# Kernel tuning notes

Measured on AMD Instinct MI355X. Metric: run time of the kernel, lower is better.

The kernel has to match this reference:

```python
import jax, jax.numpy as jnp
import numpy as np

H, I, C, B, T = 128, 270, 3, 1024, 270


def setup_inputs() -> dict:
    key = jax.random.key(0)
    ks = jax.random.split(key, 6)
    inp = {
        "x": jax.random.normal(ks[0], (B, T, I), dtype=jnp.float32),
        "Wf": jax.random.normal(ks[1], (H, I + H), dtype=jnp.float32) * 0.01,
        "Wi": jax.random.normal(ks[2], (H, I + H), dtype=jnp.float32) * 0.01,
        "Wc": jax.random.normal(ks[3], (H, I + H), dtype=jnp.float32) * 0.01,
        "Wo": jax.random.normal(ks[4], (H, I + H), dtype=jnp.float32) * 0.01,
        "Wy": jax.random.normal(ks[5], (C, H), dtype=jnp.float32) * 0.01,
        "bf": jnp.zeros((H,), jnp.float32),
        "bi": jnp.zeros((H,), jnp.float32),
        "bc": jnp.zeros((H,), jnp.float32),
        "bo": jnp.zeros((H,), jnp.float32),
        "by": jnp.zeros((C,), jnp.float32),
    }
    return inp


def _lstm_forward(x, Wf, Wi, Wc, Wo, Wy, bf, bi, bc, bo, by):
    # combined = [h_prev, x_t], so W[:, :H] acts on h, W[:, H:] acts on x.
    Wh = jnp.stack([Wf[:, :H], Wi[:, :H], Wc[:, :H], Wo[:, :H]])      # [4,H,H]
    Wx = jnp.stack([Wf[:, H:], Wi[:, H:], Wc[:, H:], Wo[:, H:]])      # [4,H,I]
    b = jnp.stack([bf, bi, bc, bo])                                   # [4,H]
    # Precompute input projections for all timesteps: one big GEMM.
    xp = jnp.einsum('bti,ghi->tbgh', x, Wx)                           # [T,B,4,H]

    def step(carry, xpt):
        h, c = carry
        pre = xpt + jnp.einsum('bh,gkh->bgk', h, Wh) + b              # [B,4,H]
        f = jax.nn.sigmoid(pre[:, 0])
        i = jax.nn.sigmoid(pre[:, 1])
        g = jnp.tanh(pre[:, 2])
        o = jax.nn.sigmoid(pre[:, 3])
        c_new = f * c + i * g
        h_new = o * jnp.tanh(c_new)
        return (h_new, c_new), h_new

    h0 = jnp.zeros((x.shape[0], H), x.dtype)
    c0 = jnp.zeros((x.shape[0], H), x.dtype)
    _, hs = jax.lax.scan(step, (h0, c0), xp)                          # hs: [T,B,H]
    all_hiddens = jnp.transpose(hs, (1, 0, 2))                        # [B,T,H]
    logits = jnp.einsum('bth,ch->btc', all_hiddens, Wy) + by
    all_outputs = jax.nn.softmax(logits, axis=-1)                     # [B,T,C]
    return all_hiddens, all_outputs


def reference(x, Wf, Wi, Wc, Wo, Wy, bf, bi, bc, bo, by):
    return _lstm_forward(x, Wf, Wi, Wc, Wo, Wy, bf, bi, bc, bo, by)
```

## Files before the change

kernel.cpp:

```cpp
#include <hip/hip_runtime.h>
#include <stdint.h>


typedef __attribute__((ext_vector_type(8))) short short8;
typedef __attribute__((ext_vector_type(4))) float f32x4;
typedef __attribute__((ext_vector_type(2))) float f32x2;
typedef __attribute__((ext_vector_type(4))) unsigned int uint4v;
typedef __attribute__((ext_vector_type(2))) unsigned int u32x2;
typedef unsigned short ush;

#define LOG2E 1.4426950408889634f
#define TWOLOG2E 2.8853900817779268f

__device__ __forceinline__ ush f2bf(float f) {
    unsigned u = __float_as_uint(f);
    return (ush)((u + 0x7FFFu + ((u >> 16) & 1u)) >> 16);
}
__device__ __forceinline__ void lds_barrier() {
    asm volatile("s_waitcnt lgkmcnt(0)" ::: "memory");
    __builtin_amdgcn_s_barrier();
    __builtin_amdgcn_sched_barrier(0);
    asm volatile("" ::: "memory");
}

__global__ __launch_bounds__(256) void pack_w(
    const float* __restrict__ Wf, const float* __restrict__ Wi,
    const float* __restrict__ Wc, const float* __restrict__ Wo,
    const float* __restrict__ bf_, const float* __restrict__ bi_,
    const float* __restrict__ bc_, const float* __restrict__ bo_,
    ush* __restrict__ Wxp, ush* __restrict__ Whp, float* __restrict__ bpk)
{
    int idx = blockIdx.x * 256 + threadIdx.x;
    if (idx < 512 * 288) {
        int u = idx / 288, i = idx - u * 288;
        int g = u >> 7, j = u & 127;
        const float* Wg = (g == 0) ? Wf : (g == 1) ? Wi : (g == 2) ? Wc : Wo;
        float v = (i < 270) ? Wg[(size_t)j * 398 + 128 + i] * LOG2E : 0.f;
        Wxp[idx] = f2bf(v);
    }
    if (idx < 512 * 128) {
        int u = idx >> 7, k = idx & 127;
        int g = u >> 7, j = u & 127;
        const float* Wg = (g == 0) ? Wf : (g == 1) ? Wi : (g == 2) ? Wc : Wo;
        Whp[idx] = f2bf(Wg[(size_t)j * 398 + k] * LOG2E);
    }
    if (idx < 512) {
        int g = idx >> 7, j = idx & 127;
        const float* bg = (g == 0) ? bf_ : (g == 1) ? bi_ : (g == 2) ? bc_ : bo_;
        bpk[idx] = bg[j] * LOG2E;
    }
}

__global__ __launch_bounds__(256, 2) void xp_gemm(
    const float* __restrict__ x, const ush* __restrict__ Wxp,
    const float* __restrict__ bpk, ush* __restrict__ xpc, int t0)
{
    __shared__ ush A_lds[64 * 296];
    const int tid = threadIdx.x;
    const int l = tid & 63, w = tid >> 6;
    const int l16 = l & 15, lq = l >> 4;
    const size_t row0 = (size_t)blockIdx.x * 64;

    const int srow = tid >> 2, sgrp = tid & 3;
    const int r = (int)row0 + srow;
    const int b = r & 1023, tt = (r >> 10) + t0;
    const float* xrow = x + ((size_t)b * 270 + tt) * 270;
    f32x2 stg[9][4];
    #pragma unroll
    for (int ks = 0; ks < 9; ++ks) {
        const int col = ks * 32 + sgrp * 8;
        const float* p = xrow + col;
        if (col + 8 <= 270) {
            stg[ks][0] = *(const f32x2*)p;       stg[ks][1] = *(const f32x2*)(p + 2);
            stg[ks][2] = *(const f32x2*)(p + 4); stg[ks][3] = *(const f32x2*)(p + 6);
        } else {
            float tv[8];
            #pragma unroll
            for (int j = 0; j < 8; ++j) tv[j] = (col + j < 270) ? p[j] : 0.f;
            stg[ks][0] = (f32x2){tv[0], tv[1]}; stg[ks][1] = (f32x2){tv[2], tv[3]};
            stg[ks][2] = (f32x2){tv[4], tv[5]}; stg[ks][3] = (f32x2){tv[6], tv[7]};
        }
    }

    const ush* bptr = Wxp + ((size_t)(w * 128 + l16)) * 288 + lq * 8;
    short8 bA[8], bB[8];
    #pragma unroll
    for (int nt = 0; nt < 8; ++nt) bA[nt] = *(const short8*)(bptr + nt * 4608);
    float bias_v[8];
    #pragma unroll
    for (int nt = 0; nt < 8; ++nt) bias_v[nt] = bpk[w * 128 + nt * 16 + l16];

    {
        ush* wrow = &A_lds[srow * 296 + sgrp * 8];
        #pragma unroll
        for (int ks = 0; ks < 9; ++ks) {
            uint4v o;
            #pragma unroll
            for (int p2 = 0; p2 < 4; ++p2) {
                unsigned v;
                asm("v_cvt_pk_bf16_f32 %0, %1, %2"
                    : "=v"(v) : "v"(stg[ks][p2].x), "v"(stg[ks][p2].y));
                o[p2] = v;
            }
            *(uint4v*)(wrow + ks * 32) = o;
        }
    }
    lds_barrier();

    f32x4 acc[4][8];
    #pragma unroll
    for (int mt = 0; mt < 4; ++mt)
        #pragma unroll
        for (int nt = 0; nt < 8; ++nt)
            acc[mt][nt] = (f32x4){bias_v[nt], bias_v[nt], bias_v[nt], bias_v[nt]};

    #pragma unroll
    for (int ks = 0; ks < 9; ++ks) {
        short8* cur = (ks & 1) ? bB : bA;
        short8* nxt = (ks & 1) ? bA : bB;
        if (ks + 1 < 9) {
            const ush* np = bptr + (ks + 1) * 32;
            #pragma unroll
            for (int nt = 0; nt < 8; ++nt) nxt[nt] = *(const short8*)(np + nt * 4608);
        }
        short8 afr[4];
        #pragma unroll
        for (int mt = 0; mt < 4; ++mt)
            afr[mt] = *(const short8*)(&A_lds[(mt * 16 + l16) * 296 + ks * 32 + lq * 8]);
        #pragma unroll
        for (int mt = 0; mt < 4; ++mt)
            #pragma unroll
            for (int nt = 0; nt < 8; ++nt)
                acc[mt][nt] = __builtin_amdgcn_mfma_f32_16x16x32_bf16(
                    afr[mt], cur[nt], acc[mt][nt], 0, 0, 0);
    }

    const int tloc = (int)(row0 >> 10);
    const int bg0 = ((int)row0 & 1023) >> 4;
    #pragma unroll
    for (int mt = 0; mt < 4; ++mt)
        #pragma unroll
        for (int nt = 0; nt < 8; ++nt) {
            int u = w * 128 + nt * 16 + l16;
            ush* dst = xpc + ((size_t)(tloc * 64 + bg0 + mt) * 512 + u) * 16 + lq * 4;
            #pragma unroll
            for (int q = 0; q < 4; ++q) dst[q] = f2bf(acc[mt][nt][q]);
        }
}

#define STEPB(T, PS, XP, CUR)                                                   \
  {                                                                             \
    const int t_ = (T);                                                         \
    const bool lw_ = (((w >> 2) ^ (t_ & 1)) == 0) && (t_ > t0);                 \
    short8 afr[4];                                                              \
    _Pragma("unroll") for (int kf = 0; kf < 4; ++kf)                            \
      afr[kf] = *(const short8*)(hbase + (CUR) * 4096 + oaf[kf]);               \
    f32x4 acc_[4];                                                              \
    _Pragma("unroll") for (int g = 0; g < 4; ++g) {                             \
      u32x2 pv_ = PS[g];                                                        \
      acc_[g][0] = __uint_as_float(pv_.x << 16);                                \
      acc_[g][1] = __uint_as_float(pv_.x & 0xffff0000u);                        \
      acc_[g][2] = __uint_as_float(pv_.y << 16);                                \
      acc_[g][3] = __uint_as_float(pv_.y & 0xffff0000u);                        \
    }                                                                           \
    if (t_ + 2 < t1) {                                                          \
      _Pragma("unroll") for (int g = 0; g < 4; ++g)                             \
        PS[g] = *(const u32x2*)((XP) + go[g]);                                  \
    }                                                                           \
    (XP) += 2 * TSTEP;                                                          \
    _Pragma("unroll") for (int kf = 0; kf < 4; ++kf)                            \
      _Pragma("unroll") for (int g = 0; g < 4; ++g)                             \
        acc_[g] = __builtin_amdgcn_mfma_f32_16x16x32_bf16(                      \
            afr[kf], whf[g][kf], acc_[g], 0, 0, 0);                             \
    f32x4 ay_ = (f32x4){0.f, 0.f, 0.f, 0.f};                                    \
    if (lw_) {                            \
      ay_ = __builtin_amdgcn_mfma_f32_16x16x32_bf16(afr[0], wyf[0], ay_, 0, 0, 0); \
      ay_ = __builtin_amdgcn_mfma_f32_16x16x32_bf16(afr[1], wyf[1], ay_, 0, 0, 0); \
      ay_ = __builtin_amdgcn_mfma_f32_16x16x32_bf16(afr[2], wyf[2], ay_, 0, 0, 0); \
      ay_ = __builtin_amdgcn_mfma_f32_16x16x32_bf16(afr[3], wyf[3], ay_, 0, 0, 0); \
    }                                                                           \
    _Pragma("unroll") for (int q = 0; q < 4; ++q) {                             \
      float pf_ = __builtin_amdgcn_fmed3f(acc_[0][q], -28.f, 28.f);             \
      float pi_ = __builtin_amdgcn_fmed3f(acc_[1][q], -28.f, 28.f);             \
      float pc2_ = __builtin_amdgcn_fmed3f(acc_[2][q] + acc_[2][q], -28.f, 28.f); \
      float po_ = __builtin_amdgcn_fmed3f(acc_[3][q], -28.f, 28.f);             \
      float ef_ = __builtin_amdgcn_exp2f(-pf_);                                 \
      float ei_ = __builtin_amdgcn_exp2f(-pi_);                                 \
      float ec2_ = __builtin_amdgcn_exp2f(-pc2_);                               \
      float eo_ = __builtin_amdgcn_exp2f(-po_);                                 \
      float df_ = 1.f + ef_;                                                    \
      float di_ = 1.f + ei_;                                                    \
      float dc_ = 1.f + ec2_;                                                   \
      float do2_ = 1.f + eo_;                                                   \
      float didc_ = di_ * dc_;                                                  \
      float num_ = c[q] * didc_ + (1.f - ec2_) * df_;                           \
      float cn_ = num_ * __builtin_amdgcn_rcpf(df_ * didc_);                    \
      c[q] = cn_;                                                               \
      float t2_ = __builtin_amdgcn_fmed3f(cn_, -10.f, 10.f);                    \
      float et2_ = __builtin_amdgcn_exp2f(-TWOLOG2E * t2_);                     \
      float hv_ = (1.f - et2_) * __builtin_amdgcn_rcpf(do2_ * (1.f + et2_));    \
      *(ush*)(hbase + ((CUR) ^ 1) * 4096 + ohw[q]) = f2bf(hv_);                 \
      *op[q] = hv_;                                                             \
      op[q] += 128;                                                             \
    }                                                                           \
    lds_barrier();                                                              \
       \
    if (lw_) {                                                                  \
      int ww_ = w & 3;                                                          \
      float L_ = ((ww_ == 0) ? ay_[0] : (ww_ == 1) ? ay_[1] : (ww_ == 2) ? ay_[2] : ay_[3]) + byl; \
      if (l16 >= 3) L_ = -1e30f;                                                \
      float m_ = fmaxf(L_, __shfl_xor(L_, 1));                                  \
      m_ = fmaxf(m_, __shfl_xor(m_, 2));                                        \
      float e_ = (l16 < 3) ? __expf(L_ - m_) : 0.f;                             \
      float s_ = e_ + __shfl_xor(e_, 1);                                        \
      s_ = s_ + __shfl_xor(s_, 2);                                              \
      if (l16 < 3)                                                              \
        out1[((size_t)(b0 + lq * 4 + ww_) * 270 + (t_ - 1)) * 3 + l16] = e_ * __builtin_amdgcn_rcpf(s_); \
    }                                                                           \
  }

__global__ __launch_bounds__(512) void lstm_scan(
    const ush* __restrict__ xpc, const ush* __restrict__ Whp,
    float* __restrict__ c_state, float* __restrict__ out0, float* __restrict__ out1,
    const float* __restrict__ Wy, const float* __restrict__ by, int t0, int t1)
{
    __shared__ ush h_lds[2][16 * 128];
    const int tid = threadIdx.x;
    const int l = tid & 63, w = tid >> 6;
    const int l16 = l & 15, lq = l >> 4;
    const int b0 = blockIdx.x * 16;
    const int jcol = w * 16 + l16;
    char* hbase = (char*)&h_lds[0][0];

    short8 whf[4][4];
    #pragma unroll
    for (int g = 0; g < 4; ++g) {
        const ush* bw = Whp + ((size_t)(g * 128 + jcol)) * 128 + lq * 8;
        #pragma unroll
        for (int kf = 0; kf < 4; ++kf) whf[g][kf] = *(const short8*)(bw + kf * 32);
    }
    short8 wyf[4];
    #pragma unroll
    for (int kf = 0; kf < 4; ++kf) {
        short8 fr;
        #pragma unroll
        for (int j = 0; j < 8; ++j)
            fr[j] = (l16 < 3) ? (short)f2bf(Wy[l16 * 128 + kf * 32 + lq * 8 + j]) : (short)0;
        wyf[kf] = fr;
    }
    const float byl = (l16 < 3) ? by[l16] : 0.f;

    int oaf[4], ohw[4];
    #pragma unroll
    for (int kf = 0; kf < 4; ++kf)
        oaf[kf] = ((l16 * 128 + kf * 32 + lq * 8) * 2) ^ ((l16 & 7) << 4);
    #pragma unroll
    for (int q = 0; q < 4; ++q) {
        int rr = lq * 4 + q;
        ohw[q] = ((rr * 128 + jcol) * 2) ^ ((rr & 7) << 4);
    }
    float* op[4];
    #pragma unroll
    for (int q = 0; q < 4; ++q)
        op[q] = out0 + (size_t)(b0 + lq * 4 + q) * (270 * 128) + (size_t)t0 * 128 + jcol;

    {
        ush* hp = &h_lds[0][0];
        for (int idx = tid; idx < 2 * 16 * 128; idx += 512) hp[idx] = 0;
    }
    __syncthreads();

    float c[4] = {0.f, 0.f, 0.f, 0.f};
    if (t0 != 0) {
        #pragma unroll
        for (int q = 0; q < 4; ++q)
            c[q] = c_state[(size_t)(b0 + lq * 4 + q) * 128 + jcol];
        for (int idx = tid; idx < 2048; idx += 512) {
            int rr = idx >> 7, k = idx & 127;
            float hvv = out0[(size_t)(b0 + rr) * (270 * 128) + (size_t)(t0 - 1) * 128 + k];
            int off = ((rr * 128 + k) * 2) ^ ((rr & 7) << 4);
            *(ush*)(hbase + off) = f2bf(hvv);
        }
        __syncthreads();
    }

    const size_t TSTEP = (size_t)64 * 512 * 16;
    const ush* xb = xpc + (size_t)blockIdx.x * 8192;
    int go[4];
    #pragma unroll
    for (int g = 0; g < 4; ++g) go[g] = (g * 128 + jcol) * 16 + lq * 4;

    u32x2 Pa[4], Pb[4];
    #pragma unroll
    for (int g = 0; g < 4; ++g) Pa[g] = *(const u32x2*)(xb + go[g]);
    #pragma unroll
    for (int g = 0; g < 4; ++g) Pb[g] = *(const u32x2*)(xb + TSTEP + go[g]);
    const ush* xpa = xb + 2 * TSTEP;
    const ush* xpb = xb + 3 * TSTEP;

    for (int t = t0; t < t1; t += 2) {
        STEPB(t, Pa, xpa, 0)
        STEPB(t + 1, Pb, xpb, 1)
    }

    {
        short8 afr[4];
        #pragma unroll
        for (int kf = 0; kf < 4; ++kf)
            afr[kf] = *(const short8*)(hbase + oaf[kf]);
        if (w < 4) {
            f32x4 ay = (f32x4){0.f, 0.f, 0.f, 0.f};
            ay = __builtin_amdgcn_mfma_f32_16x16x32_bf16(afr[0], wyf[0], ay, 0, 0, 0);
            ay = __builtin_amdgcn_mfma_f32_16x16x32_bf16(afr[1], wyf[1], ay, 0, 0, 0);
            ay = __builtin_amdgcn_mfma_f32_16x16x32_bf16(afr[2], wyf[2], ay, 0, 0, 0);
            ay = __builtin_amdgcn_mfma_f32_16x16x32_bf16(afr[3], wyf[3], ay, 0, 0, 0);
            float L = ((w == 0) ? ay[0] : (w == 1) ? ay[1] : (w == 2) ? ay[2] : ay[3]) + byl;
            if (l16 >= 3) L = -1e30f;
            float m = fmaxf(L, __shfl_xor(L, 1));
            m = fmaxf(m, __shfl_xor(m, 2));
            float e = (l16 < 3) ? __expf(L - m) : 0.f;
            float s = e + __shfl_xor(e, 1);
            s = s + __shfl_xor(s, 2);
            if (l16 < 3)
                out1[((size_t)(b0 + lq * 4 + w) * 270 + (t1 - 1)) * 3 + l16] =
                    e * __builtin_amdgcn_rcpf(s);
        }
    }

    if (t1 != 270) {
        #pragma unroll
        for (int q = 0; q < 4; ++q)
            c_state[(size_t)(b0 + lq * 4 + q) * 128 + jcol] = c[q];
    }
}

extern "C" void kernel_launch(void* const* d_in, const int* in_sizes, int n_in,
                              void* d_out, int out_size, void* d_ws, size_t ws_size,
                              hipStream_t stream) {
    (void)in_sizes; (void)n_in; (void)out_size;
    const float* x   = (const float*)d_in[0];
    const float* Wf  = (const float*)d_in[1];
    const float* Wi  = (const float*)d_in[2];
    const float* Wc  = (const float*)d_in[3];
    const float* Wo  = (const float*)d_in[4];
    const float* Wy  = (const float*)d_in[5];
    const float* bfp = (const float*)d_in[6];
    const float* bip = (const float*)d_in[7];
    const float* bcp = (const float*)d_in[8];
    const float* bop = (const float*)d_in[9];
    const float* byp = (const float*)d_in[10];

    float* out0 = (float*)d_out;
    float* out1 = out0 + (size_t)1024 * 270 * 128;

    long tc = 6;
    {
        const long cand[6] = {270, 90, 54, 30, 18, 6};
        for (int i = 0; i < 6; ++i) {
            size_t need = (size_t)cand[i] * 1048576u + (2u << 20);
            if (need <= ws_size) { tc = cand[i]; break; }
        }
    }
    char* wsb = (char*)d_ws;
    ush* xpc = (ush*)wsb;
    char* fx = wsb + (size_t)tc * 1048576u;
    float* c_state = (float*)fx;
    ush* Wxp = (ush*)(fx + 524288);
    ush* Whp = (ush*)(fx + 524288 + 294912);
    float* bpk = (float*)(fx + 524288 + 294912 + 131072);

    pack_w<<<576, 256, 0, stream>>>(Wf, Wi, Wc, Wo, bfp, bip, bcp, bop, Wxp, Whp, bpk);

    for (int t0 = 0; t0 < 270; t0 += (int)tc) {
        int Tcur = (270 - t0) < (int)tc ? (270 - t0) : (int)tc;
        int rows = Tcur * 1024;
        xp_gemm<<<rows / 64, 256, 0, stream>>>(x, Wxp, bpk, xpc, t0);
        lstm_scan<<<64, 512, 0, stream>>>(xpc, Whp, c_state, out0, out1, Wy, byp,
                                          t0, t0 + Tcur);
    }
}
```

Measured before the change: 450.8 us.

## Split LSTM scan into 8-row batch tiles across twice as many blocks

Each scan block now owns 8 batch rows instead of 16, and the launch grows from 64 to 128 blocks. The 16x16 MFMA tiles still run at full size, so half their rows are padding. Cross-half lane shuffles give each lane 2 gate elements per step instead of 4, which shortens the serial elementwise chain inside the timestep loop. The aim is to spread the latency-bound recurrence over more CUs and shorten each step, at the cost of wasted MFMA work and extra shuffles.

```diff
diff --git a/kernel.cpp b/kernel.cpp
--- a/kernel.cpp
+++ b/kernel.cpp
@@ -155,19 +155,20 @@
     short8 afr[4];                                                              \
     _Pragma("unroll") for (int kf = 0; kf < 4; ++kf)                            \
       afr[kf] = *(const short8*)(hbase + (CUR) * 4096 + oaf[kf]);               \
-    f32x4 acc_[4];                                                              \
+    float xg0_[4], xg1_[4];                                                     \
     _Pragma("unroll") for (int g = 0; g < 4; ++g) {                             \
-      u32x2 pv_ = PS[g];                                                        \
-      acc_[g][0] = __uint_as_float(pv_.x << 16);                                \
-      acc_[g][1] = __uint_as_float(pv_.x & 0xffff0000u);                        \
-      acc_[g][2] = __uint_as_float(pv_.y << 16);                                \
-      acc_[g][3] = __uint_as_float(pv_.y & 0xffff0000u);                        \
+      unsigned pv_ = PS[g];                                                     \
+      xg0_[g] = __uint_as_float(pv_ << 16);                                     \
+      xg1_[g] = __uint_as_float(pv_ & 0xffff0000u);                             \
     }                                                                           \
     if (t_ + 2 < t1) {                                                          \
       _Pragma("unroll") for (int g = 0; g < 4; ++g)                             \
-        PS[g] = *(const u32x2*)((XP) + go[g]);                                  \
+        PS[g] = *(const unsigned*)((XP) + go[g]);                               \
     }                                                                           \
     (XP) += 2 * TSTEP;                                                          \
+    f32x4 acc_[4];                                                              \
+    _Pragma("unroll") for (int g = 0; g < 4; ++g)                               \
+      acc_[g] = (f32x4){0.f, 0.f, 0.f, 0.f};                                    \
     _Pragma("unroll") for (int kf = 0; kf < 4; ++kf)                            \
       _Pragma("unroll") for (int g = 0; g < 4; ++g)                             \
         acc_[g] = __builtin_amdgcn_mfma_f32_16x16x32_bf16(                      \
@@ -179,32 +180,59 @@
       ay_ = __builtin_amdgcn_mfma_f32_16x16x32_bf16(afr[2], wyf[2], ay_, 0, 0, 0); \
       ay_ = __builtin_amdgcn_mfma_f32_16x16x32_bf16(afr[3], wyf[3], ay_, 0, 0, 0); \
     }                                                                           \
-    _Pragma("unroll") for (int q = 0; q < 4; ++q) {                             \
-      float pf_ = __builtin_amdgcn_fmed3f(acc_[0][q], -28.f, 28.f);             \
-      float pi_ = __builtin_amdgcn_fmed3f(acc_[1][q], -28.f, 28.f);             \
-      float pc2_ = __builtin_amdgcn_fmed3f(acc_[2][q] + acc_[2][q], -28.f, 28.f); \
-      float po_ = __builtin_amdgcn_fmed3f(acc_[3][q], -28.f, 28.f);             \
+     \
+    float e0_[4], e1_[4];                                                       \
+    _Pragma("unroll") for (int g = 0; g < 4; ++g) {                             \
+      float s2_ = __shfl_xor(acc_[g][2], 32);                                   \
+      float s3_ = __shfl_xor(acc_[g][3], 32);                                   \
+      e0_[g] = lo32 ? acc_[g][0] : s2_;                                         \
+      e1_[g] = lo32 ? acc_[g][1] : s3_;                                         \
+    }                                                                           \
+    float hv0_, hv1_;                                                           \
+    {                                                                           \
+      float pf_ = __builtin_amdgcn_fmed3f(e0_[0] + xg0_[0], -28.f, 28.f);       \
+      float pi_ = __builtin_amdgcn_fmed3f(e0_[1] + xg0_[1], -28.f, 28.f);       \
+      float pcs_ = e0_[2] + xg0_[2];                                            \
+      float pc2_ = __builtin_amdgcn_fmed3f(pcs_ + pcs_, -28.f, 28.f);           \
+      float po_ = __builtin_amdgcn_fmed3f(e0_[3] + xg0_[3], -28.f, 28.f);       \
       float ef_ = __builtin_amdgcn_exp2f(-pf_);                                 \
       float ei_ = __builtin_amdgcn_exp2f(-pi_);                                 \
       float ec2_ = __builtin_amdgcn_exp2f(-pc2_);                               \
       float eo_ = __builtin_amdgcn_exp2f(-po_);                                 \
       float df_ = 1.f + ef_;                                                    \
-      float di_ = 1.f + ei_;                                                    \
-      float dc_ = 1.f + ec2_;                                                   \
-      float do2_ = 1.f + eo_;                                                   \
-      float didc_ = di_ * dc_;                                                  \
-      float num_ = c[q] * didc_ + (1.f - ec2_) * df_;                           \
+      float didc_ = (1.f + ei_) * (1.f + ec2_);                                 \
+      float num_ = c0r * didc_ + (1.f - ec2_) * df_;                            \
       float cn_ = num_ * __builtin_amdgcn_rcpf(df_ * didc_);                    \
-      c[q] = cn_;                                                               \
+      c0r = cn_;                                                                \
       float t2_ = __builtin_amdgcn_fmed3f(cn_, -10.f, 10.f);                    \
       float et2_ = __builtin_amdgcn_exp2f(-TWOLOG2E * t2_);                     \
-      float hv_ = (1.f - et2_) * __builtin_amdgcn_rcpf(do2_ * (1.f + et2_));    \
-      *(ush*)(hbase + ((CUR) ^ 1) * 4096 + ohw[q]) = f2bf(hv_);                 \
-      *op[q] = hv_;                                                             \
-      op[q] += 128;                                                             \
-    }                                                                           \
+      hv0_ = (1.f - et2_) * __builtin_amdgcn_rcpf((1.f + eo_) * (1.f + et2_));  \
+    }                                                                           \
+    {                                                                           \
+      float pf_ = __builtin_amdgcn_fmed3f(e1_[0] + xg1_[0], -28.f, 28.f);       \
+      float pi_ = __builtin_amdgcn_fmed3f(e1_[1] + xg1_[1], -28.f, 28.f);       \
+      float pcs_ = e1_[2] + xg1_[2];                                            \
+      float pc2_ = __builtin_amdgcn_fmed3f(pcs_ + pcs_, -28.f, 28.f);           \
+      float po_ = __builtin_amdgcn_fmed3f(e1_[3] + xg1_[3], -28.f, 28.f);       \
+      float ef_ = __builtin_amdgcn_exp2f(-pf_);                                 \
+      float ei_ = __builtin_amdgcn_exp2f(-pi_);                                 \
+      float ec2_ = __builtin_amdgcn_exp2f(-pc2_);                               \
+      float eo_ = __builtin_amdgcn_exp2f(-po_);                                 \
+      float df_ = 1.f + ef_;                                                    \
+      float didc_ = (1.f + ei_) * (1.f + ec2_);                                 \
+      float num_ = c1r * didc_ + (1.f - ec2_) * df_;                            \
+      float cn_ = num_ * __builtin_amdgcn_rcpf(df_ * didc_);                    \
+      c1r = cn_;                                                                \
+      float t2_ = __builtin_amdgcn_fmed3f(cn_, -10.f, 10.f);                    \
+      float et2_ = __builtin_amdgcn_exp2f(-TWOLOG2E * t2_);                     \
+      hv1_ = (1.f - et2_) * __builtin_amdgcn_rcpf((1.f + eo_) * (1.f + et2_));  \
+    }                                                                           \
+    *(ush*)(hbase + ((CUR) ^ 1) * 4096 + ohw0) = f2bf(hv0_);                    \
+    *(ush*)(hbase + ((CUR) ^ 1) * 4096 + ohw1) = f2bf(hv1_);                    \
+    *op0 = hv0_; op0 += 128;                                                    \
+    *op1 = hv1_; op1 += 128;                                                    \
     lds_barrier();                                                              \
-       \
+            \
     if (lw_) {                                                                  \
       int ww_ = w & 3;                                                          \
       float L_ = ((ww_ == 0) ? ay_[0] : (ww_ == 1) ? ay_[1] : (ww_ == 2) ? ay_[2] : ay_[3]) + byl; \
@@ -214,7 +242,7 @@
       float e_ = (l16 < 3) ? __expf(L_ - m_) : 0.f;                             \
       float s_ = e_ + __shfl_xor(e_, 1);                                        \
       s_ = s_ + __shfl_xor(s_, 2);                                              \
-      if (l16 < 3)                                                              \
+      if (l16 < 3 && lq < 2)                                                    \
         out1[((size_t)(b0 + lq * 4 + ww_) * 270 + (t_ - 1)) * 3 + l16] = e_ * __builtin_amdgcn_rcpf(s_); \
     }                                                                           \
   }
@@ -228,9 +256,13 @@
     const int tid = threadIdx.x;
     const int l = tid & 63, w = tid >> 6;
     const int l16 = l & 15, lq = l >> 4;
-    const int b0 = blockIdx.x * 16;
+    const int b0 = blockIdx.x * 8;
     const int jcol = w * 16 + l16;
+    const bool lo32 = (l < 32);
     char* hbase = (char*)&h_lds[0][0];
+
+    const int row0L = lo32 ? lq * 4 : (lq - 2) * 4 + 2;
+    const int row1L = row0L + 1;
 
     short8 whf[4][4];
     #pragma unroll
@@ -250,19 +282,14 @@
     }
     const float byl = (l16 < 3) ? by[l16] : 0.f;
 
-    int oaf[4], ohw[4];
+    int oaf[4];
     #pragma unroll
     for (int kf = 0; kf < 4; ++kf)
         oaf[kf] = ((l16 * 128 + kf * 32 + lq * 8) * 2) ^ ((l16 & 7) << 4);
-    #pragma unroll
-    for (int q = 0; q < 4; ++q) {
-        int rr = lq * 4 + q;
-        ohw[q] = ((rr * 128 + jcol) * 2) ^ ((rr & 7) << 4);
-    }
-    float* op[4];
-    #pragma unroll
-    for (int q = 0; q < 4; ++q)
-        op[q] = out0 + (size_t)(b0 + lq * 4 + q) * (270 * 128) + (size_t)t0 * 128 + jcol;
+    const int ohw0 = ((row0L * 128 + jcol) * 2) ^ ((row0L & 7) << 4);
+    const int ohw1 = ((row1L * 128 + jcol) * 2) ^ ((row1L & 7) << 4);
+    float* op0 = out0 + (size_t)(b0 + row0L) * (270 * 128) + (size_t)t0 * 128 + jcol;
+    float* op1 = out0 + (size_t)(b0 + row1L) * (270 * 128) + (size_t)t0 * 128 + jcol;
 
     {
         ush* hp = &h_lds[0][0];
@@ -270,12 +297,11 @@
     }
     __syncthreads();
 
-    float c[4] = {0.f, 0.f, 0.f, 0.f};
+    float c0r = 0.f, c1r = 0.f;
     if (t0 != 0) {
-        #pragma unroll
-        for (int q = 0; q < 4; ++q)
-            c[q] = c_state[(size_t)(b0 + lq * 4 + q) * 128 + jcol];
-        for (int idx = tid; idx < 2048; idx += 512) {
+        c0r = c_state[(size_t)(b0 + row0L) * 128 + jcol];
+        c1r = c_state[(size_t)(b0 + row1L) * 128 + jcol];
+        for (int idx = tid; idx < 1024; idx += 512) {
             int rr = idx >> 7, k = idx & 127;
             float hvv = out0[(size_t)(b0 + rr) * (270 * 128) + (size_t)(t0 - 1) * 128 + k];
             int off = ((rr * 128 + k) * 2) ^ ((rr & 7) << 4);
@@ -285,16 +311,17 @@
     }
 
     const size_t TSTEP = (size_t)64 * 512 * 16;
-    const ush* xb = xpc + (size_t)blockIdx.x * 8192;
+    const ush* xb = xpc + (size_t)(blockIdx.x >> 1) * 8192;
+    const int rowbase = (b0 & 8) + row0L;
     int go[4];
     #pragma unroll
-    for (int g = 0; g < 4; ++g) go[g] = (g * 128 + jcol) * 16 + lq * 4;
-
-    u32x2 Pa[4], Pb[4];
-    #pragma unroll
-    for (int g = 0; g < 4; ++g) Pa[g] = *(const u32x2*)(xb + go[g]);
-    #pragma unroll
-    for (int g = 0; g < 4; ++g) Pb[g] = *(const u32x2*)(xb + TSTEP + go[g]);
+    for (int g = 0; g < 4; ++g) go[g] = (g * 128 + jcol) * 16 + rowbase;
+
+    unsigned Pa[4], Pb[4];
+    #pragma unroll
+    for (int g = 0; g < 4; ++g) Pa[g] = *(const unsigned*)(xb + go[g]);
+    #pragma unroll
+    for (int g = 0; g < 4; ++g) Pb[g] = *(const unsigned*)(xb + TSTEP + go[g]);
     const ush* xpa = xb + 2 * TSTEP;
     const ush* xpb = xb + 3 * TSTEP;
 
@@ -321,16 +348,15 @@
             float e = (l16 < 3) ? __expf(L - m) : 0.f;
             float s = e + __shfl_xor(e, 1);
             s = s + __shfl_xor(s, 2);
-            if (l16 < 3)
+            if (l16 < 3 && lq < 2)
                 out1[((size_t)(b0 + lq * 4 + w) * 270 + (t1 - 1)) * 3 + l16] =
                     e * __builtin_amdgcn_rcpf(s);
         }
     }
 
     if (t1 != 270) {
-        #pragma unroll
-        for (int q = 0; q < 4; ++q)
-            c_state[(size_t)(b0 + lq * 4 + q) * 128 + jcol] = c[q];
+        c_state[(size_t)(b0 + row0L) * 128 + jcol] = c0r;
+        c_state[(size_t)(b0 + row1L) * 128 + jcol] = c1r;
     }
 }
 
@@ -375,7 +401,7 @@
         int Tcur = (270 - t0) < (int)tc ? (270 - t0) : (int)tc;
         int rows = Tcur * 1024;
         xp_gemm<<<rows / 64, 256, 0, stream>>>(x, Wxp, bpk, xpc, t0);
-        lstm_scan<<<64, 512, 0, stream>>>(xpc, Whp, c_state, out0, out1, Wy, byp,
-                                          t0, t0 + Tcur);
-    }
-}
+        lstm_scan<<<128, 512, 0, stream>>>(xpc, Whp, c_state, out0, out1, Wy, byp,
+                                           t0, t0 + Tcur);
+    }
+}
```

Result: slower. 478.2 us (+6.1%).
